# Kernel optimization log

Measured on AMD Instinct MI355X. Metric: run time of the kernel, lower is better.

The kernel has to match this reference:

```python
import jax, jax.numpy as jnp
import numpy as np

# ---- static config (mirrors GptOssDecoderLayer init) ----
H = 1024      # hidden_size
HD = 64       # head_size
NQ = 16       # num_query_heads
NKV = 4       # num_key_value_heads
G = NQ // NKV # num_key_value_groups
E = 8         # num_experts
TOPK = 2      # experts_per_token
FFN = 1024    # expert intermediate (== hidden in GPT-OSS)
B, Q = 4, 128 # batch sequences, new query tokens per sequence
P, PS = 8, 128
S = P * PS    # kv length per sequence
T = B * Q     # total query tokens
SW = 128      # sliding window (layer_idx % 2 == 0 -> active)
LIMIT = 7.0   # swiglu_limit
ALPHA = 1.702
EPS = 1e-5
NEG = -1e30
SCALE = HD ** -0.5


def rmsnorm(x, w):
    return x * w * jax.lax.rsqrt(jnp.mean(x * x, axis=-1, keepdims=True) + EPS)


def setup_inputs() -> dict:
    key = jax.random.key(0)
    ks = jax.random.split(key, 16)
    hidden = jax.random.normal(ks[0], (T, H), jnp.float32)
    kv_cache = jax.random.normal(ks[1], (B * P, 2, PS, NKV, HD), jnp.float32)
    kv_page_indices = jnp.arange(B * P, dtype=jnp.int32).reshape(B, P)
    # additive causal mask: query q sits at absolute position S - Q + q
    qpos = S - Q + jnp.arange(Q)
    kpos = jnp.arange(S)
    causal = qpos[:, None] >= kpos[None, :]
    attention_mask = jnp.broadcast_to(
        jnp.where(causal, 0.0, NEG).astype(jnp.float32), (B, Q, S))
    sinks = 0.1 * jax.random.normal(ks[2], (NQ,), jnp.float32)
    w_qkv = jax.random.normal(ks[3], (H, HD * (NQ + 2 * NKV)), jnp.float32) / np.sqrt(H)
    b_qkv = jnp.zeros((HD * (NQ + 2 * NKV),), jnp.float32)
    w_o = jax.random.normal(ks[4], (NQ * HD, H), jnp.float32) / np.sqrt(NQ * HD)
    b_o = jnp.zeros((H,), jnp.float32)
    ln1_w = jnp.ones((H,), jnp.float32)
    ln2_w = jnp.ones((H,), jnp.float32)
    w_router = jax.random.normal(ks[5], (H, E), jnp.float32) / np.sqrt(H)
    b_router = jnp.zeros((E,), jnp.float32)
    w_gate_up = jax.random.normal(ks[6], (E, H, 2 * FFN), jnp.float32) / np.sqrt(H)
    b_gate_up = jnp.zeros((E, 2 * FFN), jnp.float32)
    w_down = jax.random.normal(ks[7], (E, FFN, H), jnp.float32) / np.sqrt(FFN)
    b_down = jnp.zeros((E, H), jnp.float32)
    return dict(hidden=hidden, kv_cache=kv_cache, attention_mask=attention_mask,
                kv_page_indices=kv_page_indices, sinks=sinks, w_qkv=w_qkv,
                b_qkv=b_qkv, w_o=w_o, b_o=b_o, ln1_w=ln1_w, ln2_w=ln2_w,
                w_router=w_router, b_router=b_router, w_gate_up=w_gate_up,
                b_gate_up=b_gate_up, w_down=w_down, b_down=b_down)


def reference(hidden, kv_cache, attention_mask, kv_page_indices, sinks,
              w_qkv, b_qkv, w_o, b_o, ln1_w, ln2_w, w_router, b_router,
              w_gate_up, b_gate_up, w_down, b_down):
    # ---- attention block ----
    x = rmsnorm(hidden, ln1_w)
    qkv = x @ w_qkv + b_qkv                       # [T, HD*(NQ+2*NKV)]
    q = qkv[:, :NQ * HD].reshape(B, Q, NQ, HD)
    k_new = qkv[:, NQ * HD:(NQ + NKV) * HD].reshape(B, Q, NKV, HD)
    v_new = qkv[:, (NQ + NKV) * HD:].reshape(B, Q, NKV, HD)
    # gather paged KV cache -> [B, S, NKV, HD]; write new tokens into tail slots
    pages = kv_cache[kv_page_indices]             # [B, P, 2, PS, NKV, HD]
    K = pages[:, :, 0].reshape(B, S, NKV, HD).at[:, S - Q:].set(k_new)
    V = pages[:, :, 1].reshape(B, S, NKV, HD).at[:, S - Q:].set(v_new)
    Kr = jnp.repeat(K, G, axis=2)                 # GQA expand -> [B, S, NQ, HD]
    Vr = jnp.repeat(V, G, axis=2)
    scores = jnp.einsum('bqhd,bshd->bhqs', q * SCALE, Kr) + attention_mask[:, None]
    # sliding-window (module trims pages outside the window; equivalent mask)
    qpos = S - Q + jnp.arange(Q)
    kpos = jnp.arange(S)
    win_ok = (qpos[:, None] - kpos[None, :]) < SW
    scores = jnp.where(win_ok[None, None], scores, NEG)
    m = jnp.max(scores, axis=-1)
    m = jnp.where(jnp.isinf(m) & (m < 0), 0.0, m)
    p = jnp.exp(scores - m[..., None])            # [B, NQ, Q, S]
    # attention sink joins the softmax denominator (online-softmax correction)
    denom = jnp.sum(p, axis=-1) + jnp.exp(sinks[None, :, None] - m)
    attn = jnp.einsum('bhqs,bshd->bhqd', p, Vr) / denom[..., None]
    attn = attn.transpose(0, 2, 1, 3).reshape(T, NQ * HD)
    h = hidden + attn @ w_o + b_o
    # ---- MoE block ----
    x2 = rmsnorm(h, ln2_w)
    logits = x2 @ w_router + b_router             # [T, E]
    vals, idx = jax.lax.top_k(logits, TOPK)
    wts = jax.nn.softmax(vals, axis=-1)
    comb = jnp.sum(jax.nn.one_hot(idx, E, dtype=x2.dtype) * wts[..., None], axis=1)
    gu = jnp.einsum('th,ehf->etf', x2, w_gate_up) + b_gate_up[:, None, :]
    gate = jnp.minimum(gu[..., 0::2], LIMIT)
    up = jnp.clip(gu[..., 1::2], -LIMIT, LIMIT)
    glu = gate * jax.nn.sigmoid(gate * ALPHA)
    eo = jnp.einsum('etf,efh->eth', (up + 1.0) * glu, w_down) + b_down[:, None, :]
    moe = jnp.einsum('te,eth->th', comb, eo)
    return h + moe
```

## Files before the change

kernel.cpp:

```cpp
#include <hip/hip_runtime.h>

constexpr int H    = 1024;
constexpr int HD   = 64;
constexpr int NQ   = 16;
constexpr int NKV  = 4;
constexpr int E_   = 8;
constexpr int FFN  = 1024;
constexpr int B_   = 4;
constexpr int Q_   = 128;
constexpr int P_   = 8;
constexpr int PS   = 128;
constexpr int S_   = P_ * PS;
constexpr int T_   = B_ * Q_;
constexpr int QKV_N = HD * (NQ + 2 * NKV);
constexpr float EPS   = 1e-5f;
constexpr float ALPHA = 1.702f;
constexpr float LIMIT = 7.0f;
constexpr float SCALE = 0.125f;

constexpr int MAXROWS = 1536;

typedef __attribute__((ext_vector_type(4))) float f32x4;
typedef __attribute__((ext_vector_type(8))) short s16x8;

__device__ __forceinline__ unsigned short f2bf(float f) {
    unsigned u = __float_as_uint(f);
    u += 0x7FFFu + ((u >> 16) & 1u);
    return (unsigned short)(u >> 16);
}

__global__ __launch_bounds__(256) void rmsnorm_kernel(const float* __restrict__ in,
                                                      const float* __restrict__ w,
                                                      unsigned short* __restrict__ outb,
                                                      int* __restrict__ cnt) {
    int t   = blockIdx.x;
    int tid = threadIdx.x;
    if (t == 0 && tid < E_) cnt[tid] = 0;
    float4 v = ((const float4*)(in + (size_t)t * H))[tid];
    float ss = v.x * v.x + v.y * v.y + v.z * v.z + v.w * v.w;
#pragma unroll
    for (int off = 32; off; off >>= 1) ss += __shfl_down(ss, off);
    __shared__ float partial[4];
    __shared__ float s_inv;
    if ((tid & 63) == 0) partial[tid >> 6] = ss;
    __syncthreads();
    if (tid == 0)
        s_inv = rsqrtf((partial[0] + partial[1] + partial[2] + partial[3]) * (1.0f / H) + EPS);
    __syncthreads();
    float inv = s_inv;
    float4 wv = ((const float4*)w)[tid];
    ushort4 ob;
    ob.x = f2bf(v.x * wv.x * inv); ob.y = f2bf(v.y * wv.y * inv);
    ob.z = f2bf(v.z * wv.z * inv); ob.w = f2bf(v.w * wv.w * inv);
    ((ushort4*)(outb + (size_t)t * H))[tid] = ob;
}

__global__ __launch_bounds__(256) void gemm_splitk_f32b(const unsigned short* __restrict__ Abf,
                                                        const float* __restrict__ W,
                                                        const float* __restrict__ bias,
                                                        const float* __restrict__ resid,
                                                        float* __restrict__ C,
                                                        float* __restrict__ Cdup, int N) {
    int tid = threadIdx.x;
    int wv = tid >> 6, lane = tid & 63;
    int nb16 = blockIdx.x, mb = blockIdx.y * 64;
    int r16 = lane & 15, kq = lane >> 4;
    const unsigned short* ap = Abf + (size_t)(mb + r16) * 1024 + wv * 256 + kq * 8;
    const float* wp = W + (size_t)(wv * 256 + kq * 8) * N + nb16 * 16 + r16;
    f32x4 acc[4] = {};
#pragma unroll 4
    for (int s = 0; s < 8; s++) {
        s16x8 bf;
#pragma unroll
        for (int j = 0; j < 8; j++)
            bf[j] = (short)f2bf(wp[(size_t)(s * 32 + j) * N]);
        s16x8 af[4];
#pragma unroll
        for (int mt = 0; mt < 4; mt++)
            af[mt] = *(const s16x8*)(ap + mt * 16 * 1024 + s * 32);
#pragma unroll
        for (int mt = 0; mt < 4; mt++)
            acc[mt] = __builtin_amdgcn_mfma_f32_16x16x32_bf16(af[mt], bf, acc[mt], 0, 0, 0);
    }
    __shared__ float red[4][4][4][64];
#pragma unroll
    for (int mt = 0; mt < 4; mt++)
#pragma unroll
        for (int r = 0; r < 4; r++) red[wv][mt][r][lane] = acc[mt][r];
    __syncthreads();
    int mt = tid >> 6, li = tid & 63;
    int kq2 = li >> 4, c16 = li & 15;
    int col = nb16 * 16 + c16;
    float bcol = bias[col];
#pragma unroll
    for (int r = 0; r < 4; r++) {
        float s = red[0][mt][r][li] + red[1][mt][r][li] + red[2][mt][r][li] + red[3][mt][r][li];
        int row = mb + mt * 16 + kq2 * 4 + r;
        float v = s + bcol;
        if (resid) v += resid[(size_t)row * N + col];
        C[(size_t)row * N + col] = v;
        if (Cdup) Cdup[(size_t)row * N + col] = v;
    }
}

__global__ __launch_bounds__(256) void attn_group_kernel(const float* __restrict__ qkv,
                                                         const float* __restrict__ kv_cache,
                                                         const int* __restrict__ page_idx,
                                                         const float* __restrict__ sinks,
                                                         unsigned short* __restrict__ attn_bf) {
    int blk = blockIdx.x;
    int kvh = blk & 3;
    int q   = (blk >> 2) & 127;
    int b   = blk >> 9;
    int t   = b * Q_ + q;
    int tid = threadIdx.x;
    int s_lo = S_ - Q_ - 127 + q;

    __shared__ __align__(16) float Vs[128][64];
    __shared__ __align__(16) float qs4[4][64];
    __shared__ float pv[4][128];
    __shared__ float sD[4];

#pragma unroll
    for (int r = 0; r < 8; r++) {
        int l = r * 256 + tid;
        int key = l >> 4, c = l & 15;
        int s = s_lo + key;
        const float* vp;
        if (s < S_ - Q_) {
            int page = page_idx[b * P_ + (s >> 7)];
            vp = kv_cache + (size_t)page * 65536 + 32768 + (size_t)(s & 127) * (NKV * HD) + kvh * HD;
        } else {
            vp = qkv + (size_t)(b * Q_ + (s - (S_ - Q_))) * QKV_N + (NQ + NKV) * HD + kvh * HD;
        }
        ((float4*)Vs[key])[c] = *(const float4*)(vp + c * 4);
    }
    {
        int hh = tid >> 6, d2 = tid & 63;
        qs4[hh][d2] = qkv[(size_t)t * QKV_N + (kvh * 4 + hh) * HD + d2];
    }
    __syncthreads();

    {
        int key = tid & 127, hp = tid >> 7;
        int s = s_lo + key;
        const float* kp;
        if (s < S_ - Q_) {
            int page = page_idx[b * P_ + (s >> 7)];
            kp = kv_cache + (size_t)page * 65536 + (size_t)(s & 127) * (NKV * HD) + kvh * HD;
        } else {
            kp = qkv + (size_t)(b * Q_ + (s - (S_ - Q_))) * QKV_N + NQ * HD + kvh * HD;
        }
        const float4* kp4 = (const float4*)kp;
        const float4* q0p = (const float4*)qs4[hp * 2];
        const float4* q1p = (const float4*)qs4[hp * 2 + 1];
        float sc0 = 0.f, sc1 = 0.f;
#pragma unroll
        for (int d4 = 0; d4 < 16; d4++) {
            float4 kk = kp4[d4];
            float4 q0 = q0p[d4], q1 = q1p[d4];
            sc0 += q0.x * kk.x + q0.y * kk.y + q0.z * kk.z + q0.w * kk.w;
            sc1 += q1.x * kk.x + q1.y * kk.y + q1.z * kk.z + q1.w * kk.w;
        }
        pv[hp * 2][key]     = sc0 * SCALE;
        pv[hp * 2 + 1][key] = sc1 * SCALE;
    }
    __syncthreads();

    {
        int wv = tid >> 6, lane = tid & 63;
        float a0 = pv[wv][lane], a1 = pv[wv][lane + 64];
        float m = fmaxf(a0, a1);
#pragma unroll
        for (int off = 32; off; off >>= 1) m = fmaxf(m, __shfl_xor(m, off));
        float p0 = __expf(a0 - m), p1 = __expf(a1 - m);
        float l = p0 + p1;
#pragma unroll
        for (int off = 32; off; off >>= 1) l += __shfl_xor(l, off);
        pv[wv][lane] = p0;
        pv[wv][lane + 64] = p1;
        if (lane == 0) sD[wv] = l + __expf(sinks[kvh * 4 + wv] - m);
    }
    __syncthreads();

    {
        int hh = tid >> 6, d2 = tid & 63;
        float a0 = 0.f, a1 = 0.f, a2 = 0.f, a3 = 0.f;
#pragma unroll 4
        for (int i = 0; i < 128; i += 4) {
            a0 += pv[hh][i]     * Vs[i][d2];
            a1 += pv[hh][i + 1] * Vs[i + 1][d2];
            a2 += pv[hh][i + 2] * Vs[i + 2][d2];
            a3 += pv[hh][i + 3] * Vs[i + 3][d2];
        }
        float acc = ((a0 + a1) + (a2 + a3)) / sD[hh];
        attn_bf[(size_t)t * (NQ * HD) + (kvh * 4 + hh) * HD + d2] = f2bf(acc);
    }
}

__global__ __launch_bounds__(256) void rms_router_kernel(const float* __restrict__ hbuf,
                                                         const float* __restrict__ ln2w,
                                                         const float* __restrict__ w_router,
                                                         const float* __restrict__ b_router,
                                                         unsigned short* __restrict__ x2bf,
                                                         int* __restrict__ ridx,
                                                         float* __restrict__ rwt,
                                                         int* __restrict__ cnt) {
    int t = blockIdx.x;
    int tid = threadIdx.x;
    float4 v = ((const float4*)(hbuf + (size_t)t * H))[tid];
    float ss = v.x * v.x + v.y * v.y + v.z * v.z + v.w * v.w;
#pragma unroll
    for (int off = 32; off; off >>= 1) ss += __shfl_down(ss, off);
    __shared__ float partial[4];
    __shared__ float s_inv;
    if ((tid & 63) == 0) partial[tid >> 6] = ss;
    __syncthreads();
    if (tid == 0)
        s_inv = rsqrtf((partial[0] + partial[1] + partial[2] + partial[3]) * (1.0f / H) + EPS);
    __syncthreads();
    float inv = s_inv;
    float4 wv = ((const float4*)ln2w)[tid];
    float4 o;
    o.x = v.x * wv.x * inv; o.y = v.y * wv.y * inv;
    o.z = v.z * wv.z * inv; o.w = v.w * wv.w * inv;
    ushort4 ob;
    ob.x = f2bf(o.x); ob.y = f2bf(o.y); ob.z = f2bf(o.z); ob.w = f2bf(o.w);
    ((ushort4*)(x2bf + (size_t)t * H))[tid] = ob;

    const float4* wr = (const float4*)(w_router + (size_t)tid * 4 * E_);
    float p[E_];
    {
        float4 r0a = wr[0], r0b = wr[1];
        float4 r1a = wr[2], r1b = wr[3];
        float4 r2a = wr[4], r2b = wr[5];
        float4 r3a = wr[6], r3b = wr[7];
        p[0] = o.x * r0a.x + o.y * r1a.x + o.z * r2a.x + o.w * r3a.x;
        p[1] = o.x * r0a.y + o.y * r1a.y + o.z * r2a.y + o.w * r3a.y;
        p[2] = o.x * r0a.z + o.y * r1a.z + o.z * r2a.z + o.w * r3a.z;
        p[3] = o.x * r0a.w + o.y * r1a.w + o.z * r2a.w + o.w * r3a.w;
        p[4] = o.x * r0b.x + o.y * r1b.x + o.z * r2b.x + o.w * r3b.x;
        p[5] = o.x * r0b.y + o.y * r1b.y + o.z * r2b.y + o.w * r3b.y;
        p[6] = o.x * r0b.z + o.y * r1b.z + o.z * r2b.z + o.w * r3b.z;
        p[7] = o.x * r0b.w + o.y * r1b.w + o.z * r2b.w + o.w * r3b.w;
    }
    __shared__ float wsum[4][E_];
    int wv2 = tid >> 6, lane = tid & 63;
#pragma unroll
    for (int e = 0; e < E_; e++) {
        float r = p[e];
#pragma unroll
        for (int off = 32; off; off >>= 1) r += __shfl_xor(r, off);
        if (lane == 0) wsum[wv2][e] = r;
    }
    __syncthreads();
    __shared__ float logits[E_];
    if (tid < E_)
        logits[tid] = wsum[0][tid] + wsum[1][tid] + wsum[2][tid] + wsum[3][tid] + b_router[tid];
    __syncthreads();
    if (tid == 0) {
        int i0 = 0; float v0 = logits[0];
        for (int ee = 1; ee < E_; ee++)
            if (logits[ee] > v0) { v0 = logits[ee]; i0 = ee; }
        int i1 = -1; float v1 = -3.4e38f;
        for (int ee = 0; ee < E_; ee++)
            if (ee != i0 && logits[ee] > v1) { v1 = logits[ee]; i1 = ee; }
        float w0 = 1.0f / (1.0f + __expf(v1 - v0));
        ridx[t * 2] = i0; ridx[t * 2 + 1] = i1;
        rwt[t * 2] = w0;  rwt[t * 2 + 1] = 1.0f - w0;
        atomicAdd(&cnt[i0], 1);
        atomicAdd(&cnt[i1], 1);
    }
}

__global__ __launch_bounds__(256) void plumb_kernel(const int* __restrict__ cnt,
                                                    const int* __restrict__ ridx,
                                                    int* __restrict__ poff,
                                                    int* __restrict__ list) {
    __shared__ int lpos[E_], lpoff[E_];
    int tid = threadIdx.x;
    if (tid == 0) {
        int run = 0;
        for (int e = 0; e < E_; e++) { lpoff[e] = run; poff[e] = run; run += (cnt[e] + 63) & ~63; }
    }
    if (tid < E_) lpos[tid] = 0;
    __syncthreads();
    for (int i = tid; i < 2 * T_; i += 256) {
        int e = ridx[i];
        int pp = atomicAdd(&lpos[e], 1);
        list[lpoff[e] + pp] = i;
    }
}

__global__ __launch_bounds__(256) void moe_gateup_sk(const unsigned short* __restrict__ x2bf,
                                                     const int* __restrict__ list,
                                                     const int* __restrict__ cnt,
                                                     const int* __restrict__ poff,
                                                     const float* __restrict__ wgu,
                                                     const float* __restrict__ b_gate_up,
                                                     unsigned short* __restrict__ act_bf) {
    int e  = blockIdx.y >> 3;
    int tl = blockIdx.y & 7;
    int n  = cnt[e];
    if (tl * 128 >= n) return;
    int base = poff[e];
    int nb = blockIdx.x;

    int tid = threadIdx.x;
    int wv = tid >> 6, lane = tid & 63;
    int r16 = lane & 15, kq = lane >> 4;
    const unsigned short* ap[8];
#pragma unroll
    for (int mt = 0; mt < 8; mt++) {
        int row = tl * 128 + mt * 16 + r16;
        int t2 = (row < n) ? list[base + row] : 0;
        ap[mt] = x2bf + (size_t)(t2 >> 1) * 1024 + wv * 256 + kq * 8;
    }
    const float* wp = wgu + ((size_t)e * 1024 + wv * 256 + kq * 8) * 2048 + 2 * (nb * 16 + r16);

    f32x4 accg[8] = {}, accu[8] = {};
#pragma unroll 2
    for (int s = 0; s < 8; s++) {
        s16x8 bg, bu;
#pragma unroll
        for (int j = 0; j < 8; j++) {
            float2 v = *(const float2*)(wp + (size_t)(s * 32 + j) * 2048);
            bg[j] = (short)f2bf(v.x);
            bu[j] = (short)f2bf(v.y);
        }
#pragma unroll
        for (int mt = 0; mt < 8; mt++) {
            s16x8 af = *(const s16x8*)(ap[mt] + s * 32);
            accg[mt] = __builtin_amdgcn_mfma_f32_16x16x32_bf16(af, bg, accg[mt], 0, 0, 0);
            accu[mt] = __builtin_amdgcn_mfma_f32_16x16x32_bf16(af, bu, accu[mt], 0, 0, 0);
        }
    }
    __shared__ float redg[4][4][4][64];
    __shared__ float redu[4][4][4][64];
    int col = nb * 16 + (tid & 15);
    float bg_b = b_gate_up[(size_t)e * 2048 + 2 * col];
    float bu_b = b_gate_up[(size_t)e * 2048 + 2 * col + 1];
#pragma unroll
    for (int h = 0; h < 2; h++) {
        __syncthreads();
#pragma unroll
        for (int m2 = 0; m2 < 4; m2++)
#pragma unroll
            for (int r = 0; r < 4; r++) {
                redg[wv][m2][r][lane] = accg[h * 4 + m2][r];
                redu[wv][m2][r][lane] = accu[h * 4 + m2][r];
            }
        __syncthreads();
        int m2 = tid >> 6, li = tid & 63;
        int kq2 = li >> 4;
#pragma unroll
        for (int r = 0; r < 4; r++) {
            int rr = tl * 128 + (h * 4 + m2) * 16 + kq2 * 4 + r;
            if (rr < n) {
                float g = redg[0][m2][r][li] + redg[1][m2][r][li] + redg[2][m2][r][li] + redg[3][m2][r][li];
                float u = redu[0][m2][r][li] + redu[1][m2][r][li] + redu[2][m2][r][li] + redu[3][m2][r][li];
                float gate = fminf(g + bg_b, LIMIT);
                float up2 = fminf(fmaxf(u + bu_b, -LIMIT), LIMIT);
                float glu = gate / (1.0f + __expf(-ALPHA * gate));
                act_bf[(size_t)(base + rr) * FFN + col] = f2bf((up2 + 1.0f) * glu);
            }
        }
    }
}

__global__ __launch_bounds__(256) void moe_down_sk(const unsigned short* __restrict__ act_bf,
                                                   const int* __restrict__ list,
                                                   const int* __restrict__ cnt,
                                                   const int* __restrict__ poff,
                                                   const float* __restrict__ rwt,
                                                   const float* __restrict__ wdn,
                                                   const float* __restrict__ b_down,
                                                   float* __restrict__ out) {
    int e  = blockIdx.y >> 3;
    int tl = blockIdx.y & 7;
    int n  = cnt[e];
    if (tl * 128 >= n) return;
    int base = poff[e];
    int nb = blockIdx.x;

    int tid = threadIdx.x;
    int wv = tid >> 6, lane = tid & 63;
    int r16 = lane & 15, kq = lane >> 4;
    const unsigned short* ap = act_bf + (size_t)(base + tl * 128 + r16) * 1024 + wv * 256 + kq * 8;
    const float* wp = wdn + (size_t)e * FFN * H + (size_t)(wv * 256 + kq * 8) * 1024 + nb * 16 + r16;

    f32x4 acc[8] = {};
#pragma unroll 2
    for (int s = 0; s < 8; s++) {
        s16x8 bf;
#pragma unroll
        for (int j = 0; j < 8; j++)
            bf[j] = (short)f2bf(wp[(size_t)(s * 32 + j) * 1024]);
#pragma unroll
        for (int mt = 0; mt < 8; mt++) {
            s16x8 af = *(const s16x8*)(ap + mt * 16 * 1024 + s * 32);
            acc[mt] = __builtin_amdgcn_mfma_f32_16x16x32_bf16(af, bf, acc[mt], 0, 0, 0);
        }
    }
    __shared__ float red[4][4][4][64];
    int col = nb * 16 + (tid & 15);
    float bcol = b_down[(size_t)e * 1024 + col];
#pragma unroll
    for (int h = 0; h < 2; h++) {
        __syncthreads();
#pragma unroll
        for (int m2 = 0; m2 < 4; m2++)
#pragma unroll
            for (int r = 0; r < 4; r++) red[wv][m2][r][lane] = acc[h * 4 + m2][r];
        __syncthreads();
        int m2 = tid >> 6, li = tid & 63;
        int kq2 = li >> 4;
#pragma unroll
        for (int r = 0; r < 4; r++) {
            int rr = tl * 128 + (h * 4 + m2) * 16 + kq2 * 4 + r;
            if (rr < n) {
                float s = red[0][m2][r][li] + red[1][m2][r][li] + red[2][m2][r][li] + red[3][m2][r][li];
                int t2 = list[base + rr];
                atomicAdd(&out[(size_t)(t2 >> 1) * H + col], rwt[t2] * (s + bcol));
            }
        }
    }
}

extern "C" void kernel_launch(void* const* d_in, const int* in_sizes, int n_in,
                              void* d_out, int out_size, void* d_ws, size_t ws_size,
                              hipStream_t stream) {
    const float* hidden          = (const float*)d_in[0];
    const float* kv_cache        = (const float*)d_in[1];
    const int*   kv_page_indices = (const int*)d_in[3];
    const float* sinks           = (const float*)d_in[4];
    const float* w_qkv           = (const float*)d_in[5];
    const float* b_qkv           = (const float*)d_in[6];
    const float* w_o             = (const float*)d_in[7];
    const float* b_o             = (const float*)d_in[8];
    const float* ln1_w           = (const float*)d_in[9];
    const float* ln2_w           = (const float*)d_in[10];
    const float* w_router        = (const float*)d_in[11];
    const float* b_router        = (const float*)d_in[12];
    const float* w_gate_up       = (const float*)d_in[13];
    const float* b_gate_up       = (const float*)d_in[14];
    const float* w_down          = (const float*)d_in[15];
    const float* b_down          = (const float*)d_in[16];
    float* out = (float*)d_out;

    char* base = (char*)d_ws;
    float* qkv   = (float*)base;                       base += (size_t)T_ * QKV_N * 4;
    float* hbuf  = (float*)base;                       base += (size_t)T_ * H * 4;
    unsigned short* x_bf    = (unsigned short*)base;   base += (size_t)T_ * H * 2;
    unsigned short* x2_bf   = (unsigned short*)base;   base += (size_t)T_ * H * 2;
    unsigned short* attn_bf = (unsigned short*)base;   base += (size_t)T_ * NQ * HD * 2;
    unsigned short* act_bf  = (unsigned short*)base;   base += (size_t)(MAXROWS + 128) * FFN * 2;
    float* rwt  = (float*)base;                        base += 2 * T_ * 4;
    int*   ridx = (int*)base;                          base += 2 * T_ * 4;
    int*   cnt  = (int*)base;                          base += E_ * 4;
    int*   poff = (int*)base;                          base += E_ * 4;
    int*   list = (int*)base;                          base += MAXROWS * 4;

    rmsnorm_kernel<<<T_, 256, 0, stream>>>(hidden, ln1_w, x_bf, cnt);
    gemm_splitk_f32b<<<dim3(QKV_N / 16, T_ / 64), 256, 0, stream>>>(
        x_bf, w_qkv, b_qkv, nullptr, qkv, nullptr, QKV_N);
    attn_group_kernel<<<B_ * Q_ * NKV, 256, 0, stream>>>(qkv, kv_cache, kv_page_indices, sinks, attn_bf);
    gemm_splitk_f32b<<<dim3(H / 16, T_ / 64), 256, 0, stream>>>(
        attn_bf, w_o, b_o, hidden, hbuf, out, H);
    rms_router_kernel<<<T_, 256, 0, stream>>>(hbuf, ln2_w, w_router, b_router,
                                              x2_bf, ridx, rwt, cnt);
    plumb_kernel<<<1, 256, 0, stream>>>(cnt, ridx, poff, list);
    moe_gateup_sk<<<dim3(FFN / 16, E_ * 8), 256, 0, stream>>>(
        x2_bf, list, cnt, poff, w_gate_up, b_gate_up, act_bf);
    moe_down_sk<<<dim3(H / 16, E_ * 8), 256, 0, stream>>>(
        act_bf, list, cnt, poff, rwt, w_down, b_down, out);
}
```

Before: 312.4 us.

## Stage bf16 weight tiles in LDS with double buffering across all GEMMs

Replaces the intra-block split-K GEMMs, where each wave covered a K quarter and partials were reduced through shared memory, with full-K tiles. Each block converts a 64x32 weight slab to bf16 into a double-buffered LDS tile, and the next slab's global loads are issued while MFMAs run on the current one. Weight fp32 loads become coalesced 32-wide rows, each weight is converted once per block instead of once per wave, and the LDS reduction is gone. The gate/up kernel now pairs interleaved gate/up columns with a lane shuffle. The down projection adds a 2-way K split via grid z with atomics, which doubles atomic traffic to the output.

```diff
diff --git a/kernel.cpp b/kernel.cpp
--- a/kernel.cpp
+++ b/kernel.cpp
@@ -55,51 +55,76 @@
     ((ushort4*)(outb + (size_t)t * H))[tid] = ob;
 }
 
-__global__ __launch_bounds__(256) void gemm_splitk_f32b(const unsigned short* __restrict__ Abf,
-                                                        const float* __restrict__ W,
-                                                        const float* __restrict__ bias,
-                                                        const float* __restrict__ resid,
-                                                        float* __restrict__ C,
-                                                        float* __restrict__ Cdup, int N) {
-    int tid = threadIdx.x;
-    int wv = tid >> 6, lane = tid & 63;
-    int nb16 = blockIdx.x, mb = blockIdx.y * 64;
+__global__ __launch_bounds__(256) void gemm_dense_t(const unsigned short* __restrict__ Abf,
+                                                    const float* __restrict__ W,
+                                                    const float* __restrict__ bias,
+                                                    const float* __restrict__ resid,
+                                                    float* __restrict__ C,
+                                                    float* __restrict__ Cdup, int N) {
+    int nb = blockIdx.x, mb = blockIdx.y * 64;
+    int tid = threadIdx.x;
+    int w = tid >> 6, lane = tid & 63;
     int r16 = lane & 15, kq = lane >> 4;
-    const unsigned short* ap = Abf + (size_t)(mb + r16) * 1024 + wv * 256 + kq * 8;
-    const float* wp = W + (size_t)(wv * 256 + kq * 8) * N + nb16 * 16 + r16;
-    f32x4 acc[4] = {};
-#pragma unroll 4
-    for (int s = 0; s < 8; s++) {
-        s16x8 bf;
-#pragma unroll
-        for (int j = 0; j < 8; j++)
-            bf[j] = (short)f2bf(wp[(size_t)(s * 32 + j) * N]);
-        s16x8 af[4];
-#pragma unroll
-        for (int mt = 0; mt < 4; mt++)
-            af[mt] = *(const s16x8*)(ap + mt * 16 * 1024 + s * 32);
-#pragma unroll
-        for (int mt = 0; mt < 4; mt++)
-            acc[mt] = __builtin_amdgcn_mfma_f32_16x16x32_bf16(af[mt], bf, acc[mt], 0, 0, 0);
-    }
-    __shared__ float red[4][4][4][64];
-#pragma unroll
-    for (int mt = 0; mt < 4; mt++)
-#pragma unroll
-        for (int r = 0; r < 4; r++) red[wv][mt][r][lane] = acc[mt][r];
-    __syncthreads();
-    int mt = tid >> 6, li = tid & 63;
-    int kq2 = li >> 4, c16 = li & 15;
-    int col = nb16 * 16 + c16;
-    float bcol = bias[col];
-#pragma unroll
-    for (int r = 0; r < 4; r++) {
-        float s = red[0][mt][r][li] + red[1][mt][r][li] + red[2][mt][r][li] + red[3][mt][r][li];
-        int row = mb + mt * 16 + kq2 * 4 + r;
-        float v = s + bcol;
-        if (resid) v += resid[(size_t)row * N + col];
-        C[(size_t)row * N + col] = v;
-        if (Cdup) Cdup[(size_t)row * N + col] = v;
+    int skb = tid >> 5, sn = tid & 31;
+
+    __shared__ unsigned short Wt[2][8][32][8];
+
+    size_t sN = (size_t)N;
+    const float* wsrc = W + (size_t)(skb * 8) * sN + nb * 32 + sn;
+    const unsigned short* ap = Abf + (size_t)(mb + w * 16 + r16) * 1024 + kq * 8;
+
+    f32x4 acc[2] = {};
+    float wr[8];
+#pragma unroll
+    for (int j = 0; j < 8; j++) wr[j] = wsrc[(size_t)j * sN];
+    {
+        s16x8 p;
+#pragma unroll
+        for (int j = 0; j < 8; j++) p[j] = (short)f2bf(wr[j]);
+        *(s16x8*)&Wt[0][skb][sn][0] = p;
+    }
+    __syncthreads();
+
+#pragma unroll 2
+    for (int t = 0; t < 16; t++) {
+        s16x8 af[2];
+#pragma unroll
+        for (int ks = 0; ks < 2; ks++)
+            af[ks] = *(const s16x8*)(ap + t * 64 + ks * 32);
+        if (t < 15) {
+            const float* ws = wsrc + (size_t)(t + 1) * 64 * sN;
+#pragma unroll
+            for (int j = 0; j < 8; j++) wr[j] = ws[(size_t)j * sN];
+        }
+#pragma unroll
+        for (int ks = 0; ks < 2; ks++) {
+            s16x8 b0 = *(const s16x8*)&Wt[t & 1][ks * 4 + kq][r16][0];
+            s16x8 b1 = *(const s16x8*)&Wt[t & 1][ks * 4 + kq][16 + r16][0];
+            acc[0] = __builtin_amdgcn_mfma_f32_16x16x32_bf16(af[ks], b0, acc[0], 0, 0, 0);
+            acc[1] = __builtin_amdgcn_mfma_f32_16x16x32_bf16(af[ks], b1, acc[1], 0, 0, 0);
+        }
+        if (t < 15) {
+            s16x8 p;
+#pragma unroll
+            for (int j = 0; j < 8; j++) p[j] = (short)f2bf(wr[j]);
+            *(s16x8*)&Wt[(t & 1) ^ 1][skb][sn][0] = p;
+        }
+        __syncthreads();
+    }
+
+    int row0 = mb + w * 16 + kq * 4;
+#pragma unroll
+    for (int nf = 0; nf < 2; nf++) {
+        int col = nb * 32 + nf * 16 + r16;
+        float bcol = bias[col];
+#pragma unroll
+        for (int r = 0; r < 4; r++) {
+            int row = row0 + r;
+            float v = acc[nf][r] + bcol;
+            if (resid) v += resid[(size_t)row * sN + col];
+            C[(size_t)row * sN + col] = v;
+            if (Cdup) Cdup[(size_t)row * sN + col] = v;
+        }
     }
 }
 
@@ -292,139 +317,190 @@
     }
 }
 
-__global__ __launch_bounds__(256) void moe_gateup_sk(const unsigned short* __restrict__ x2bf,
-                                                     const int* __restrict__ list,
-                                                     const int* __restrict__ cnt,
-                                                     const int* __restrict__ poff,
-                                                     const float* __restrict__ wgu,
-                                                     const float* __restrict__ b_gate_up,
-                                                     unsigned short* __restrict__ act_bf) {
-    int e  = blockIdx.y >> 3;
-    int tl = blockIdx.y & 7;
-    int n  = cnt[e];
+__global__ __launch_bounds__(256) void moe_gateup_t(const unsigned short* __restrict__ x2bf,
+                                                    const int* __restrict__ list,
+                                                    const int* __restrict__ cnt,
+                                                    const int* __restrict__ poff,
+                                                    const float* __restrict__ wgu,
+                                                    const float* __restrict__ bgu,
+                                                    unsigned short* __restrict__ act_bf) {
+    int e = blockIdx.y >> 3, tl = blockIdx.y & 7;
+    int n = cnt[e];
     if (tl * 128 >= n) return;
     int base = poff[e];
     int nb = blockIdx.x;
-
-    int tid = threadIdx.x;
-    int wv = tid >> 6, lane = tid & 63;
+    int tid = threadIdx.x;
+    int w = tid >> 6, lane = tid & 63;
     int r16 = lane & 15, kq = lane >> 4;
-    const unsigned short* ap[8];
-#pragma unroll
-    for (int mt = 0; mt < 8; mt++) {
-        int row = tl * 128 + mt * 16 + r16;
-        int t2 = (row < n) ? list[base + row] : 0;
-        ap[mt] = x2bf + (size_t)(t2 >> 1) * 1024 + wv * 256 + kq * 8;
-    }
-    const float* wp = wgu + ((size_t)e * 1024 + wv * 256 + kq * 8) * 2048 + 2 * (nb * 16 + r16);
-
-    f32x4 accg[8] = {}, accu[8] = {};
+    int skb = tid >> 5, sn = tid & 31;
+
+    __shared__ unsigned short Wt[2][8][32][8];
+
+    const float* wsrc = wgu + (size_t)e * (1024 * 2048) + (size_t)(skb * 8) * 2048 + nb * 32 + sn;
+
+    const unsigned short* ap[2];
+#pragma unroll
+    for (int mf = 0; mf < 2; mf++) {
+        int rr = tl * 128 + w * 32 + mf * 16 + r16;
+        int t2 = (rr < n) ? list[base + rr] : list[base];
+        ap[mf] = x2bf + (size_t)(t2 >> 1) * 1024 + kq * 8;
+    }
+
+    f32x4 acc[2][2] = {};
+    float wr[8];
+#pragma unroll
+    for (int j = 0; j < 8; j++) wr[j] = wsrc[(size_t)j * 2048];
+    {
+        s16x8 p;
+#pragma unroll
+        for (int j = 0; j < 8; j++) p[j] = (short)f2bf(wr[j]);
+        *(s16x8*)&Wt[0][skb][sn][0] = p;
+    }
+    __syncthreads();
+
 #pragma unroll 2
-    for (int s = 0; s < 8; s++) {
-        s16x8 bg, bu;
-#pragma unroll
-        for (int j = 0; j < 8; j++) {
-            float2 v = *(const float2*)(wp + (size_t)(s * 32 + j) * 2048);
-            bg[j] = (short)f2bf(v.x);
-            bu[j] = (short)f2bf(v.y);
-        }
-#pragma unroll
-        for (int mt = 0; mt < 8; mt++) {
-            s16x8 af = *(const s16x8*)(ap[mt] + s * 32);
-            accg[mt] = __builtin_amdgcn_mfma_f32_16x16x32_bf16(af, bg, accg[mt], 0, 0, 0);
-            accu[mt] = __builtin_amdgcn_mfma_f32_16x16x32_bf16(af, bu, accu[mt], 0, 0, 0);
-        }
-    }
-    __shared__ float redg[4][4][4][64];
-    __shared__ float redu[4][4][4][64];
-    int col = nb * 16 + (tid & 15);
-    float bg_b = b_gate_up[(size_t)e * 2048 + 2 * col];
-    float bu_b = b_gate_up[(size_t)e * 2048 + 2 * col + 1];
-#pragma unroll
-    for (int h = 0; h < 2; h++) {
+    for (int t = 0; t < 16; t++) {
+        s16x8 af[2][2];
+#pragma unroll
+        for (int mf = 0; mf < 2; mf++)
+#pragma unroll
+            for (int ks = 0; ks < 2; ks++)
+                af[mf][ks] = *(const s16x8*)(ap[mf] + t * 64 + ks * 32);
+        if (t < 15) {
+            const float* ws = wsrc + (size_t)(t + 1) * 64 * 2048;
+#pragma unroll
+            for (int j = 0; j < 8; j++) wr[j] = ws[(size_t)j * 2048];
+        }
+#pragma unroll
+        for (int ks = 0; ks < 2; ks++) {
+            s16x8 b0 = *(const s16x8*)&Wt[t & 1][ks * 4 + kq][r16][0];
+            s16x8 b1 = *(const s16x8*)&Wt[t & 1][ks * 4 + kq][16 + r16][0];
+#pragma unroll
+            for (int mf = 0; mf < 2; mf++) {
+                acc[mf][0] = __builtin_amdgcn_mfma_f32_16x16x32_bf16(af[mf][ks], b0, acc[mf][0], 0, 0, 0);
+                acc[mf][1] = __builtin_amdgcn_mfma_f32_16x16x32_bf16(af[mf][ks], b1, acc[mf][1], 0, 0, 0);
+            }
+        }
+        if (t < 15) {
+            s16x8 p;
+#pragma unroll
+            for (int j = 0; j < 8; j++) p[j] = (short)f2bf(wr[j]);
+            *(s16x8*)&Wt[(t & 1) ^ 1][skb][sn][0] = p;
+        }
         __syncthreads();
-#pragma unroll
-        for (int m2 = 0; m2 < 4; m2++)
+    }
+
+    int parity = r16 & 1;
+#pragma unroll
+    for (int mf = 0; mf < 2; mf++)
+#pragma unroll
+        for (int nf = 0; nf < 2; nf++) {
+            int gucol = nb * 32 + nf * 16 + r16;
+            float bb = bgu[(size_t)e * 2048 + gucol];
 #pragma unroll
             for (int r = 0; r < 4; r++) {
-                redg[wv][m2][r][lane] = accg[h * 4 + m2][r];
-                redu[wv][m2][r][lane] = accu[h * 4 + m2][r];
+                float v = acc[mf][nf][r] + bb;
+                float o = __shfl_xor(v, 1);
+                if (!parity) {
+                    float g = fminf(v, LIMIT);
+                    float u = fminf(fmaxf(o, -LIMIT), LIMIT);
+                    float glu = g / (1.0f + __expf(-ALPHA * g));
+                    int rr = tl * 128 + w * 32 + mf * 16 + kq * 4 + r;
+                    if (rr < n)
+                        act_bf[(size_t)(base + rr) * FFN + (gucol >> 1)] = f2bf((u + 1.0f) * glu);
+                }
             }
-        __syncthreads();
-        int m2 = tid >> 6, li = tid & 63;
-        int kq2 = li >> 4;
-#pragma unroll
-        for (int r = 0; r < 4; r++) {
-            int rr = tl * 128 + (h * 4 + m2) * 16 + kq2 * 4 + r;
-            if (rr < n) {
-                float g = redg[0][m2][r][li] + redg[1][m2][r][li] + redg[2][m2][r][li] + redg[3][m2][r][li];
-                float u = redu[0][m2][r][li] + redu[1][m2][r][li] + redu[2][m2][r][li] + redu[3][m2][r][li];
-                float gate = fminf(g + bg_b, LIMIT);
-                float up2 = fminf(fmaxf(u + bu_b, -LIMIT), LIMIT);
-                float glu = gate / (1.0f + __expf(-ALPHA * gate));
-                act_bf[(size_t)(base + rr) * FFN + col] = f2bf((up2 + 1.0f) * glu);
-            }
-        }
-    }
-}
-
-__global__ __launch_bounds__(256) void moe_down_sk(const unsigned short* __restrict__ act_bf,
-                                                   const int* __restrict__ list,
-                                                   const int* __restrict__ cnt,
-                                                   const int* __restrict__ poff,
-                                                   const float* __restrict__ rwt,
-                                                   const float* __restrict__ wdn,
-                                                   const float* __restrict__ b_down,
-                                                   float* __restrict__ out) {
-    int e  = blockIdx.y >> 3;
-    int tl = blockIdx.y & 7;
-    int n  = cnt[e];
+        }
+}
+
+__global__ __launch_bounds__(256) void moe_down_t(const unsigned short* __restrict__ act_bf,
+                                                  const int* __restrict__ list,
+                                                  const int* __restrict__ cnt,
+                                                  const int* __restrict__ poff,
+                                                  const float* __restrict__ rwt,
+                                                  const float* __restrict__ wdn,
+                                                  const float* __restrict__ b_down,
+                                                  float* __restrict__ out) {
+    int e = blockIdx.y >> 3, tl = blockIdx.y & 7;
+    int n = cnt[e];
     if (tl * 128 >= n) return;
     int base = poff[e];
     int nb = blockIdx.x;
-
-    int tid = threadIdx.x;
-    int wv = tid >> 6, lane = tid & 63;
+    int z  = blockIdx.z;
+    int tid = threadIdx.x;
+    int w = tid >> 6, lane = tid & 63;
     int r16 = lane & 15, kq = lane >> 4;
-    const unsigned short* ap = act_bf + (size_t)(base + tl * 128 + r16) * 1024 + wv * 256 + kq * 8;
-    const float* wp = wdn + (size_t)e * FFN * H + (size_t)(wv * 256 + kq * 8) * 1024 + nb * 16 + r16;
-
-    f32x4 acc[8] = {};
+    int skb = tid >> 5, sn = tid & 31;
+
+    __shared__ unsigned short Wt[2][8][32][8];
+
+    const float* wsrc = wdn + (size_t)e * (1024 * 1024) + (size_t)(z * 512 + skb * 8) * 1024 + nb * 32 + sn;
+    const unsigned short* ap[2];
+#pragma unroll
+    for (int mf = 0; mf < 2; mf++)
+        ap[mf] = act_bf + (size_t)(base + tl * 128 + w * 32 + mf * 16 + r16) * 1024 + z * 512 + kq * 8;
+
+    f32x4 acc[2][2] = {};
+    float wr[8];
+#pragma unroll
+    for (int j = 0; j < 8; j++) wr[j] = wsrc[(size_t)j * 1024];
+    {
+        s16x8 p;
+#pragma unroll
+        for (int j = 0; j < 8; j++) p[j] = (short)f2bf(wr[j]);
+        *(s16x8*)&Wt[0][skb][sn][0] = p;
+    }
+    __syncthreads();
+
 #pragma unroll 2
-    for (int s = 0; s < 8; s++) {
-        s16x8 bf;
-#pragma unroll
-        for (int j = 0; j < 8; j++)
-            bf[j] = (short)f2bf(wp[(size_t)(s * 32 + j) * 1024]);
-#pragma unroll
-        for (int mt = 0; mt < 8; mt++) {
-            s16x8 af = *(const s16x8*)(ap + mt * 16 * 1024 + s * 32);
-            acc[mt] = __builtin_amdgcn_mfma_f32_16x16x32_bf16(af, bf, acc[mt], 0, 0, 0);
-        }
-    }
-    __shared__ float red[4][4][4][64];
-    int col = nb * 16 + (tid & 15);
-    float bcol = b_down[(size_t)e * 1024 + col];
-#pragma unroll
-    for (int h = 0; h < 2; h++) {
+    for (int t = 0; t < 8; t++) {
+        s16x8 af[2][2];
+#pragma unroll
+        for (int mf = 0; mf < 2; mf++)
+#pragma unroll
+            for (int ks = 0; ks < 2; ks++)
+                af[mf][ks] = *(const s16x8*)(ap[mf] + t * 64 + ks * 32);
+        if (t < 7) {
+            const float* ws = wsrc + (size_t)(t + 1) * 64 * 1024;
+#pragma unroll
+            for (int j = 0; j < 8; j++) wr[j] = ws[(size_t)j * 1024];
+        }
+#pragma unroll
+        for (int ks = 0; ks < 2; ks++) {
+            s16x8 b0 = *(const s16x8*)&Wt[t & 1][ks * 4 + kq][r16][0];
+            s16x8 b1 = *(const s16x8*)&Wt[t & 1][ks * 4 + kq][16 + r16][0];
+#pragma unroll
+            for (int mf = 0; mf < 2; mf++) {
+                acc[mf][0] = __builtin_amdgcn_mfma_f32_16x16x32_bf16(af[mf][ks], b0, acc[mf][0], 0, 0, 0);
+                acc[mf][1] = __builtin_amdgcn_mfma_f32_16x16x32_bf16(af[mf][ks], b1, acc[mf][1], 0, 0, 0);
+            }
+        }
+        if (t < 7) {
+            s16x8 p;
+#pragma unroll
+            for (int j = 0; j < 8; j++) p[j] = (short)f2bf(wr[j]);
+            *(s16x8*)&Wt[(t & 1) ^ 1][skb][sn][0] = p;
+        }
         __syncthreads();
-#pragma unroll
-        for (int m2 = 0; m2 < 4; m2++)
-#pragma unroll
-            for (int r = 0; r < 4; r++) red[wv][m2][r][lane] = acc[h * 4 + m2][r];
-        __syncthreads();
-        int m2 = tid >> 6, li = tid & 63;
-        int kq2 = li >> 4;
+    }
+
+#pragma unroll
+    for (int mf = 0; mf < 2; mf++)
 #pragma unroll
         for (int r = 0; r < 4; r++) {
-            int rr = tl * 128 + (h * 4 + m2) * 16 + kq2 * 4 + r;
+            int rr = tl * 128 + w * 32 + mf * 16 + kq * 4 + r;
             if (rr < n) {
-                float s = red[0][m2][r][li] + red[1][m2][r][li] + red[2][m2][r][li] + red[3][m2][r][li];
                 int t2 = list[base + rr];
-                atomicAdd(&out[(size_t)(t2 >> 1) * H + col], rwt[t2] * (s + bcol));
+                float sc = rwt[t2];
+                float* op = out + (size_t)(t2 >> 1) * H;
+#pragma unroll
+                for (int nf = 0; nf < 2; nf++) {
+                    int col = nb * 32 + nf * 16 + r16;
+                    float v = acc[mf][nf][r] + (z == 0 ? b_down[(size_t)e * 1024 + col] : 0.0f);
+                    atomicAdd(op + col, sc * v);
+                }
             }
         }
-    }
 }
 
 extern "C" void kernel_launch(void* const* d_in, const int* in_sizes, int n_in,
@@ -462,16 +538,16 @@
     int*   list = (int*)base;                          base += MAXROWS * 4;
 
     rmsnorm_kernel<<<T_, 256, 0, stream>>>(hidden, ln1_w, x_bf, cnt);
-    gemm_splitk_f32b<<<dim3(QKV_N / 16, T_ / 64), 256, 0, stream>>>(
+    gemm_dense_t<<<dim3(QKV_N / 32, T_ / 64), 256, 0, stream>>>(
         x_bf, w_qkv, b_qkv, nullptr, qkv, nullptr, QKV_N);
     attn_group_kernel<<<B_ * Q_ * NKV, 256, 0, stream>>>(qkv, kv_cache, kv_page_indices, sinks, attn_bf);
-    gemm_splitk_f32b<<<dim3(H / 16, T_ / 64), 256, 0, stream>>>(
+    gemm_dense_t<<<dim3(H / 32, T_ / 64), 256, 0, stream>>>(
         attn_bf, w_o, b_o, hidden, hbuf, out, H);
     rms_router_kernel<<<T_, 256, 0, stream>>>(hbuf, ln2_w, w_router, b_router,
                                               x2_bf, ridx, rwt, cnt);
     plumb_kernel<<<1, 256, 0, stream>>>(cnt, ridx, poff, list);
-    moe_gateup_sk<<<dim3(FFN / 16, E_ * 8), 256, 0, stream>>>(
+    moe_gateup_t<<<dim3(FFN * 2 / 32, E_ * 8), 256, 0, stream>>>(
         x2_bf, list, cnt, poff, w_gate_up, b_gate_up, act_bf);
-    moe_down_sk<<<dim3(H / 16, E_ * 8), 256, 0, stream>>>(
+    moe_down_t<<<dim3(H / 32, E_ * 8, 2), 256, 0, stream>>>(
         act_bf, list, cnt, poff, rwt, w_down, b_down, out);
 }
```

Result: slower. 335.4 us (+7.3%).
